# Optimization experiments

Measured on AMD Instinct MI355X. Metric: run time of the kernel, lower is better.

## Reference

```python
import jax, jax.numpy as jnp
import numpy as np

D_MODEL = 1024
N_HEADS = 16
D_FF = 4096
EPS = 1e-6


def _linear_params(key, d_in, d_out):
    kw, kb = jax.random.split(key)
    bound = 1.0 / np.sqrt(d_in)
    W = jax.random.uniform(kw, (d_out, d_in), minval=-bound, maxval=bound, dtype=jnp.float32)
    b = jax.random.uniform(kb, (d_out,), minval=-bound, maxval=bound, dtype=jnp.float32)
    return W, b


def setup_inputs() -> dict:
    key = jax.random.key(0)
    keys = jax.random.split(key, 8)
    x = jax.random.normal(keys[0], (4, 2048, D_MODEL), dtype=jnp.float32)
    mask = jnp.ones((4, 1, 1, 2048), dtype=jnp.bool_)
    Wq, bq = _linear_params(keys[1], D_MODEL, D_MODEL)
    Wk, bk = _linear_params(keys[2], D_MODEL, D_MODEL)
    Wv, bv = _linear_params(keys[3], D_MODEL, D_MODEL)
    Wo, bo = _linear_params(keys[4], D_MODEL, D_MODEL)
    W1, b1 = _linear_params(keys[5], D_MODEL, D_FF)
    W2, b2 = _linear_params(keys[6], D_FF, D_MODEL)
    ln1_g = jnp.ones((D_MODEL,), jnp.float32); ln1_b = jnp.zeros((D_MODEL,), jnp.float32)
    ln2_g = jnp.ones((D_MODEL,), jnp.float32); ln2_b = jnp.zeros((D_MODEL,), jnp.float32)
    return {"x": x, "mask": mask,
            "Wq": Wq, "bq": bq, "Wk": Wk, "bk": bk, "Wv": Wv, "bv": bv,
            "Wo": Wo, "bo": bo, "W1": W1, "b1": b1, "W2": W2, "b2": b2,
            "ln1_g": ln1_g, "ln1_b": ln1_b, "ln2_g": ln2_g, "ln2_b": ln2_b}


def _layernorm(x, g, b):
    # torch LayerNorm here uses unbiased std and divides by (std + eps)
    mean = jnp.mean(x, axis=-1, keepdims=True)
    std = jnp.std(x, axis=-1, keepdims=True, ddof=1)
    return g * (x - mean) / (std + EPS) + b


def _gelu_tanh(x):
    c = np.sqrt(2.0 / np.pi).astype(np.float32)
    return 0.5 * x * (1.0 + jnp.tanh(c * (x + 0.044715 * x * x * x)))


def _mha(xn, mask, Wq, bq, Wk, bk, Wv, bv, Wo, bo):
    B, S, D = xn.shape
    d_k = D // N_HEADS
    def proj(W, b):
        y = jnp.einsum('bsd,ed->bse', xn, W) + b
        return y.reshape(B, S, N_HEADS, d_k).transpose(0, 2, 1, 3)  # [B,h,S,d_k]
    q, k, v = proj(Wq, bq), proj(Wk, bk), proj(Wv, bv)
    scores = jnp.einsum('bhqd,bhkd->bhqk', q, k) / np.float32(np.sqrt(d_k))
    scores = jnp.where(mask, scores, jnp.float32(-1e9))
    p = jax.nn.softmax(scores, axis=-1)
    o = jnp.einsum('bhqk,bhkd->bhqd', p, v)
    o = o.transpose(0, 2, 1, 3).reshape(B, S, D)
    return jnp.einsum('bsd,ed->bse', o, Wo) + bo


def reference(x, mask, Wq, bq, Wk, bk, Wv, bv, Wo, bo, W1, b1, W2, b2,
              ln1_g, ln1_b, ln2_g, ln2_b):
    xn = _layernorm(x, ln1_g, ln1_b)
    y = x + _mha(xn, mask, Wq, bq, Wk, bk, Wv, bv, Wo, bo)
    yn = _layernorm(y, ln2_g, ln2_b)
    h = _gelu_tanh(jnp.einsum('bsd,fd->bsf', yn, W1) + b1)
    z = y + (jnp.einsum('bsf,df->bsd', h, W2) + b2)
    return z
```

## Files before the change

kernel.cpp:

```cpp
#include <hip/hip_runtime.h>

typedef __bf16 bf16;
typedef __bf16 bfx4 __attribute__((ext_vector_type(4)));
typedef __bf16 bfx8 __attribute__((ext_vector_type(8)));
typedef float  fx4  __attribute__((ext_vector_type(4)));

#define NTOK 8192
#define DM   1024
#define DFF  4096
#define SEQ  2048
#define NH   16
#define DK   64

#define OFF_WQKV 0ull
#define OFF_WO   (OFF_WQKV + 3072ull*1024*2)
#define OFF_W1   (OFF_WO   + 1024ull*1024*2)
#define OFF_W2   (OFF_W1   + 4096ull*1024*2)
#define OFF_BQKV (OFF_W2   + 4096ull*1024*2)
#define OFF_XN   (OFF_BQKV + 3072ull*4)
#define OFF_QKV  (OFF_XN   + 8192ull*1024*2)
#define OFF_ATTN (OFF_QKV  + 8192ull*3072*2)
#define OFF_Y    (OFF_ATTN + 8192ull*1024*2)
#define OFF_VT   OFF_Y
#define OFF_H    OFF_XN
#define OFF_YN   OFF_ATTN

__device__ __forceinline__ void gload16(const void* g, void* l) {
  __builtin_amdgcn_global_load_lds(
      (__attribute__((address_space(1))) void*)(g),
      (__attribute__((address_space(3))) void*)(l), 16, 0, 0);
}

__device__ __forceinline__ float gelu_tanh(float x) {
  float u = 0.7978845608028654f * (x + 0.044715f * x * x * x);
  float t = 1.f - 2.f / (__expf(2.f * u) + 1.f);
  return 0.5f * x * (1.f + t);
}

__global__ __launch_bounds__(256) void cast_all(const float* __restrict__ Wq,
                                                const float* __restrict__ Wk,
                                                const float* __restrict__ Wv,
                                                const float* __restrict__ Wo,
                                                const float* __restrict__ W1,
                                                const float* __restrict__ W2,
                                                bf16* __restrict__ dst) {
  const int bid = blockIdx.x;
  const int g = bid >> 9;
  const int j = ((bid & 511) << 11) + threadIdx.x * 8;
  const float* s;
  if (g == 0) s = Wq;
  else if (g == 1) s = Wk;
  else if (g == 2) s = Wv;
  else if (g == 3) s = Wo;
  else if (g < 8) s = W1 + (size_t)(g - 4) * 1048576;
  else s = W2 + (size_t)(g - 8) * 1048576;
  const float4 a = *(const float4*)(s + j);
  const float4 c = *(const float4*)(s + j + 4);
  bfx8 o;
  o[0] = (bf16)a.x; o[1] = (bf16)a.y; o[2] = (bf16)a.z; o[3] = (bf16)a.w;
  o[4] = (bf16)c.x; o[5] = (bf16)c.y; o[6] = (bf16)c.z; o[7] = (bf16)c.w;
  *(bfx8*)(dst + (size_t)g * 1048576 + j) = o;
}

__global__ void biask(const float* __restrict__ bq, const float* __restrict__ bk,
                      const float* __restrict__ bv, float* __restrict__ o) {
  const int i = blockIdx.x * 1024 + threadIdx.x;
  const float* s = blockIdx.x == 0 ? bq : (blockIdx.x == 1 ? bk : bv);
  o[i] = s[threadIdx.x];
}

__global__ __launch_bounds__(256) void ln_kernel(const float* __restrict__ x,
                                                 const float* __restrict__ g,
                                                 const float* __restrict__ b,
                                                 bf16* __restrict__ out) {
  const int row = blockIdx.x;
  const int c = threadIdx.x * 4;
  const float4 v = *(const float4*)&x[(size_t)row * DM + c];
  float s1 = v.x + v.y + v.z + v.w;
  float s2 = v.x * v.x + v.y * v.y + v.z * v.z + v.w * v.w;
  #pragma unroll
  for (int o = 32; o; o >>= 1) { s1 += __shfl_xor(s1, o); s2 += __shfl_xor(s2, o); }
  __shared__ float red[8];
  const int wid = threadIdx.x >> 6;
  if ((threadIdx.x & 63) == 0) { red[wid] = s1; red[4 + wid] = s2; }
  __syncthreads();
  s1 = red[0] + red[1] + red[2] + red[3];
  s2 = red[4] + red[5] + red[6] + red[7];
  const float mean = s1 * (1.f / (float)DM);
  const float var = (s2 - (float)DM * mean * mean) * (1.f / (float)(DM - 1));
  const float inv = 1.f / (sqrtf(fmaxf(var, 0.f)) + 1e-6f);
  bfx4 o;
  o[0] = (bf16)(g[c + 0] * (v.x - mean) * inv + b[c + 0]);
  o[1] = (bf16)(g[c + 1] * (v.y - mean) * inv + b[c + 1]);
  o[2] = (bf16)(g[c + 2] * (v.z - mean) * inv + b[c + 2]);
  o[3] = (bf16)(g[c + 3] * (v.w - mean) * inv + b[c + 3]);
  *(bfx4*)&out[(size_t)row * DM + c] = o;
}

template <int EPI, int VSPLIT>
__global__ __launch_bounds__(256, 2) void gemmk(const bf16* __restrict__ A,
                                                const bf16* __restrict__ B,
                                                const float* __restrict__ bias,
                                                const float* __restrict__ resid,
                                                bf16* __restrict__ vt,
                                                void* __restrict__ outp,
                                                int M, int N, int K) {
  extern __shared__ char lds[];
  const int tid = threadIdx.x;
  const int lane = tid & 63, w = tid >> 6;
  const int l15 = lane & 15, lhi = lane >> 4;
  const int wm = w >> 1, wn = w & 1;

  const int gy = gridDim.y;
  const int nwg = gridDim.x * gy;
  const int L = blockIdx.y * gridDim.x + blockIdx.x;
  const int wid = (L & 7) * (nwg >> 3) + (L >> 3);
  const int m0 = (wid / gy) * 256;
  const int n0 = (wid % gy) * 128;
  const size_t str = (size_t)K * 2;

  const int rT = tid >> 2;
  const int cT = ((tid & 3) ^ ((tid >> 3) & 3)) * 16;
  const char* aS = (const char*)A + (size_t)(m0 + rT) * str + cT;
  const char* bS = (const char*)B + (size_t)(n0 + rT) * str + cT;

  auto stage = [&](int buf, int kt) {
    const size_t kb = (size_t)kt * 64;
    char* d = lds + buf * 24576 + tid * 16;
    #pragma unroll
    for (int p = 0; p < 4; ++p)
      gload16(aS + (size_t)(p * 64) * str + kb, d + p * 4096);
    #pragma unroll
    for (int p = 0; p < 2; ++p)
      gload16(bS + (size_t)(p * 64) * str + kb, d + 16384 + p * 4096);
  };

  fx4 acc[8][4] = {};
  const int nK = K >> 5;

  stage(0, 0);
  stage(1, 1);

  #pragma unroll 1
  for (int t = 0; t < nK; ++t) {
    if (t < nK - 1)
      asm volatile("s_waitcnt vmcnt(6) lgkmcnt(0)" ::: "memory");
    else
      asm volatile("s_waitcnt vmcnt(0) lgkmcnt(0)" ::: "memory");
    __builtin_amdgcn_s_barrier();
    asm volatile("" ::: "memory");
    if (t + 2 < nK) stage((t + 2) % 3, t + 2);

    const char* Ab = lds + (t % 3) * 24576;
    const char* Bb = Ab + 16384;
    bfx8 af[8], bv[4];
    #pragma unroll
    for (int i = 0; i < 8; ++i) {
      const int r = wm * 128 + i * 16 + l15;
      af[i] = *(const bfx8*)(Ab + r * 64 + ((lhi * 16) ^ (((r >> 1) & 3) << 4)));
    }
    #pragma unroll
    for (int j = 0; j < 4; ++j) {
      const int r = wn * 64 + j * 16 + l15;
      bv[j] = *(const bfx8*)(Bb + r * 64 + ((lhi * 16) ^ (((r >> 1) & 3) << 4)));
    }
    __builtin_amdgcn_s_setprio(1);
    #pragma unroll
    for (int i = 0; i < 8; ++i)
      #pragma unroll
      for (int j = 0; j < 4; ++j)
        acc[i][j] = __builtin_amdgcn_mfma_f32_16x16x32_bf16(af[i], bv[j], acc[i][j], 0, 0, 0);
    __builtin_amdgcn_s_setprio(0);
  }

  const int rb = m0 + wm * 128 + lhi * 4;
  const int cb = n0 + wn * 64 + l15;
  #pragma unroll
  for (int j = 0; j < 4; ++j) {
    const int c = cb + j * 16;
    const float bvv = bias[c];
    if (VSPLIT && c >= 2048) {
      const int hd = c - 2048;
      #pragma unroll
      for (int i = 0; i < 8; ++i) {
        const int tok = rb + i * 16;
        const int bb = tok >> 11;
        bfx4 o4;
        #pragma unroll
        for (int e = 0; e < 4; ++e) o4[e] = (bf16)(acc[i][j][e] + bvv);
        *(bfx4*)&vt[((size_t)(bb * 1024 + hd)) * SEQ + (tok & 2047)] = o4;
      }
    } else {
      #pragma unroll
      for (int i = 0; i < 8; ++i) {
        #pragma unroll
        for (int e = 0; e < 4; ++e) {
          const size_t idx = (size_t)(rb + i * 16 + e) * N + c;
          float v = acc[i][j][e] + bvv;
          if constexpr (EPI == 1) v = gelu_tanh(v);
          if constexpr (EPI == 2) {
            ((float*)outp)[idx] = v + resid[idx];
          } else {
            ((bf16*)outp)[idx] = (bf16)v;
          }
        }
      }
    }
  }
}

__global__ __launch_bounds__(256, 4) void attn_kernel(const bf16* __restrict__ QKV,
                                                      const bf16* __restrict__ VT,
                                                      bf16* __restrict__ O) {
  __shared__ bf16 lds[2][2][4096];
  const int tid = threadIdx.x;
  const int lane = tid & 63, w = tid >> 6;
  const int l15 = lane & 15, lhi = lane >> 4;
  int id = blockIdx.x;
  id = (id & 7) * 128 + (id >> 3);
  const int q0 = (id & 15) * 128;
  const int h = (id >> 4) & 15;
  const int b = id >> 8;
  const size_t tokbase = (size_t)b * SEQ;

  const int lin0 = w * 1024 + lane * 16;
  const int lin1 = lin0 + 4096;
  const int row0 = lin0 >> 7, row1 = lin1 >> 7;
  const int cs0 = (lin0 & 127) ^ ((row0 & 7) << 4);
  const int cs1 = (lin1 & 127) ^ ((row1 & 7) << 4);
  const char* kp0 = (const char*)QKV + ((tokbase + row0) * 3072 + 1024 + h * 64) * 2 + cs0;
  const char* kp1 = (const char*)QKV + ((tokbase + row1) * 3072 + 1024 + h * 64) * 2 + cs1;
  const char* vbase = (const char*)(VT + (size_t)((b * NH + h) * 64) * SEQ);
  const char* vp0 = vbase + (size_t)row0 * (SEQ * 2) + cs0;
  const char* vp1 = vbase + (size_t)row1 * (SEQ * 2) + cs1;
  char* const ldsb = (char*)&lds[0][0][0];
  int dofs = 0;
  const long KADV = 64l * 3072 * 2;
  const long VADV = 64l * 2;

  auto stage = [&]() {
    gload16(kp0, ldsb + dofs + lin0);
    gload16(kp1, ldsb + dofs + lin1);
    gload16(vp0, ldsb + dofs + 8192 + lin0);
    gload16(vp1, ldsb + dofs + 8192 + lin1);
    kp0 += KADV; kp1 += KADV; vp0 += VADV; vp1 += VADV;
    dofs ^= 16384;
  };

  stage();

  bfx8 qf[2][2];
  #pragma unroll
  for (int m = 0; m < 2; ++m)
    #pragma unroll
    for (int kk = 0; kk < 2; ++kk) {
      bfx8 raw = *(const bfx8*)&QKV[(tokbase + q0 + w * 32 + m * 16 + l15) * 3072
                                    + h * DK + kk * 32 + lhi * 8];
      bfx8 sc;
      #pragma unroll
      for (int e = 0; e < 8; ++e) sc[e] = (bf16)((float)raw[e] * 0.18033688011112042f);
      qf[m][kk] = sc;
    }

  fx4 acc[2][4] = {};
  fx4 lsum[2] = {};
  bfx8 ones;
  #pragma unroll
  for (int e = 0; e < 8; ++e) ones[e] = (bf16)1.0f;

  const int NT = SEQ / 64;
  #pragma unroll 2
  for (int t = 0; t < NT; ++t) {
    if (t + 1 < NT) {
      stage();
      asm volatile("s_waitcnt vmcnt(4)" ::: "memory");
    } else {
      asm volatile("s_waitcnt vmcnt(0)" ::: "memory");
    }
    __builtin_amdgcn_s_barrier();

    const char* Kl = ldsb + ((t & 1) << 14);
    const char* Vl = Kl + 8192;

    fx4 s[2][4] = {};
    #pragma unroll
    for (int kk = 0; kk < 2; ++kk) {
      bfx8 kf[4];
      #pragma unroll
      for (int n = 0; n < 4; ++n) {
        const int row = n * 16 + l15;
        kf[n] = *(const bfx8*)(Kl + row * 128 + ((kk * 64 + lhi * 16) ^ ((row & 7) << 4)));
      }
      __builtin_amdgcn_s_setprio(1);
      #pragma unroll
      for (int m = 0; m < 2; ++m)
        #pragma unroll
        for (int n = 0; n < 4; ++n)
          s[m][n] = __builtin_amdgcn_mfma_f32_16x16x32_bf16(kf[n], qf[m][kk], s[m][n], 0, 0, 0);
      __builtin_amdgcn_s_setprio(0);
    }

    uint32_t pu[2][4][2];
    #pragma unroll
    for (int m = 0; m < 2; ++m)
      #pragma unroll
      for (int n = 0; n < 4; ++n) {
        const float p0 = exp2f(s[m][n][0]);
        const float p1 = exp2f(s[m][n][1]);
        const float p2 = exp2f(s[m][n][2]);
        const float p3 = exp2f(s[m][n][3]);
        union { bf16 h2[2]; uint32_t u; } c0, c1;
        c0.h2[0] = (bf16)p0; c0.h2[1] = (bf16)p1;
        c1.h2[0] = (bf16)p2; c1.h2[1] = (bf16)p3;
        pu[m][n][0] = c0.u; pu[m][n][1] = c1.u;
      }

    #pragma unroll
    for (int kk = 0; kk < 2; ++kk) {
      bfx8 pB[2];
      #pragma unroll
      for (int m = 0; m < 2; ++m) {
        union { uint32_t u[4]; bfx8 v; } cb2;
        cb2.u[0] = pu[m][2 * kk][0];
        cb2.u[1] = pu[m][2 * kk][1];
        cb2.u[2] = pu[m][2 * kk + 1][0];
        cb2.u[3] = pu[m][2 * kk + 1][1];
        pB[m] = cb2.v;
      }
      __builtin_amdgcn_s_setprio(1);
      #pragma unroll
      for (int m = 0; m < 2; ++m)
        lsum[m] = __builtin_amdgcn_mfma_f32_16x16x32_bf16(ones, pB[m], lsum[m], 0, 0, 0);
      __builtin_amdgcn_s_setprio(0);
      #pragma unroll
      for (int dn = 0; dn < 4; ++dn) {
        const int row = dn * 16 + l15;
        const int sw = (row & 7) << 4;
        union { bfx4 q2[2]; bfx8 v; } vv;
        vv.q2[0] = *(const bfx4*)(Vl + row * 128 + ((kk * 64 + lhi * 8) ^ sw));
        vv.q2[1] = *(const bfx4*)(Vl + row * 128 + ((kk * 64 + 32 + lhi * 8) ^ sw));
        __builtin_amdgcn_s_setprio(1);
        #pragma unroll
        for (int m = 0; m < 2; ++m)
          acc[m][dn] = __builtin_amdgcn_mfma_f32_16x16x32_bf16(vv.v, pB[m], acc[m][dn], 0, 0, 0);
        __builtin_amdgcn_s_setprio(0);
      }
    }

    asm volatile("s_waitcnt lgkmcnt(0)" ::: "memory");
    __builtin_amdgcn_s_barrier();
  }

  __syncthreads();
  bf16* Ep = &lds[0][0][0] + w * 2048;
  const float rinv0 = __builtin_amdgcn_rcpf(lsum[0][0]);
  const float rinv1 = __builtin_amdgcn_rcpf(lsum[1][0]);
  #pragma unroll
  for (int m = 0; m < 2; ++m) {
    const int qr = m * 16 + l15;
    const int sw = (qr & 7) << 4;
    const float ri = m ? rinv1 : rinv0;
    #pragma unroll
    for (int dn = 0; dn < 4; ++dn)
      #pragma unroll
      for (int e = 0; e < 4; ++e) {
        const int d = dn * 16 + lhi * 4 + e;
        *(bf16*)((char*)Ep + qr * 128 + ((2 * d) ^ sw)) = (bf16)(acc[m][dn][e] * ri);
      }
  }
  __syncthreads();
  #pragma unroll
  for (int j = 0; j < 4; ++j) {
    const int qr = lane >> 1;
    const int cbyte = (lane & 1) * 64 + j * 16;
    bfx8 v = *(const bfx8*)((char*)Ep + qr * 128 + (cbyte ^ ((qr & 7) << 4)));
    *(bfx8*)&O[(tokbase + q0 + w * 32 + qr) * (size_t)DM + h * DK + (lane & 1) * 32 + j * 8] = v;
  }
}

extern "C" void kernel_launch(void* const* d_in, const int* in_sizes, int n_in,
                              void* d_out, int out_size, void* d_ws, size_t ws_size,
                              hipStream_t stream) {
  const float* x  = (const float*)d_in[0];
  const float* Wq = (const float*)d_in[2];
  const float* bq = (const float*)d_in[3];
  const float* Wk = (const float*)d_in[4];
  const float* bk = (const float*)d_in[5];
  const float* Wv = (const float*)d_in[6];
  const float* bv = (const float*)d_in[7];
  const float* Wo = (const float*)d_in[8];
  const float* bo = (const float*)d_in[9];
  const float* W1 = (const float*)d_in[10];
  const float* b1 = (const float*)d_in[11];
  const float* W2 = (const float*)d_in[12];
  const float* b2 = (const float*)d_in[13];
  const float* g1 = (const float*)d_in[14];
  const float* be1 = (const float*)d_in[15];
  const float* g2 = (const float*)d_in[16];
  const float* be2 = (const float*)d_in[17];

  char* ws = (char*)d_ws;
  bf16* WQKVb = (bf16*)(ws + OFF_WQKV);
  bf16* WOb   = (bf16*)(ws + OFF_WO);
  bf16* W1b   = (bf16*)(ws + OFF_W1);
  bf16* W2b   = (bf16*)(ws + OFF_W2);
  float* BQKV = (float*)(ws + OFF_BQKV);
  bf16* XN    = (bf16*)(ws + OFF_XN);
  bf16* QKVb  = (bf16*)(ws + OFF_QKV);
  bf16* ATTNb = (bf16*)(ws + OFF_ATTN);
  float* Yb   = (float*)(ws + OFF_Y);
  bf16* VTb   = (bf16*)(ws + OFF_VT);
  bf16* Hb    = (bf16*)(ws + OFF_H);
  bf16* YNb   = (bf16*)(ws + OFF_YN);

  hipFuncSetAttribute((const void*)&gemmk<0, 1>,
                      hipFuncAttributeMaxDynamicSharedMemorySize, 73728);
  hipFuncSetAttribute((const void*)&gemmk<1, 0>,
                      hipFuncAttributeMaxDynamicSharedMemorySize, 73728);
  hipFuncSetAttribute((const void*)&gemmk<2, 0>,
                      hipFuncAttributeMaxDynamicSharedMemorySize, 73728);

  cast_all<<<6144, 256, 0, stream>>>(Wq, Wk, Wv, Wo, W1, W2, WQKVb);
  biask<<<3, 1024, 0, stream>>>(bq, bk, bv, BQKV);

  ln_kernel<<<NTOK, 256, 0, stream>>>(x, g1, be1, XN);
  gemmk<0, 1><<<dim3(32, 24), 256, 73728, stream>>>(XN, WQKVb, BQKV, nullptr,
                                                    VTb, QKVb, NTOK, 3072, 1024);
  attn_kernel<<<1024, 256, 0, stream>>>(QKVb, VTb, ATTNb);
  gemmk<2, 0><<<dim3(32, 8), 256, 73728, stream>>>(ATTNb, WOb, bo, x, nullptr,
                                                   Yb, NTOK, 1024, 1024);
  ln_kernel<<<NTOK, 256, 0, stream>>>(Yb, g2, be2, YNb);
  gemmk<1, 0><<<dim3(32, 32), 256, 73728, stream>>>(YNb, W1b, b1, nullptr,
                                                    nullptr, Hb, NTOK, 4096, 1024);
  gemmk<2, 0><<<dim3(32, 8), 256, 73728, stream>>>(Hb, W2b, b2, Yb, nullptr,
                                                   (float*)d_out, NTOK, 1024, 4096);
}
```

Measured before the change: 440.1 us.

## Double K tile to 64 with two-stage buffering and compile-time GEMM shapes

The GEMM K-step grows from 32 to 64 elements per stage, with an 8-way XOR swizzle over 128-byte LDS rows. It drops the three-buffer, two-ahead prefetch for two buffers with one stage in flight, and adds a second barrier per iteration. Each GEMM becomes its own kernel with constant M/N/K and launch_bounds(256,1), raising LDS per block to 96 KB. This halves loop and barrier overhead per unit of work and lets the compiler specialise the shapes, but it reduces prefetch depth and likely occupancy.

```diff
diff --git a/kernel.cpp b/kernel.cpp
--- a/kernel.cpp
+++ b/kernel.cpp
@@ -98,14 +98,13 @@
 }
 
 template <int EPI, int VSPLIT>
-__global__ __launch_bounds__(256, 2) void gemmk(const bf16* __restrict__ A,
-                                                const bf16* __restrict__ B,
-                                                const float* __restrict__ bias,
-                                                const float* __restrict__ resid,
-                                                bf16* __restrict__ vt,
-                                                void* __restrict__ outp,
-                                                int M, int N, int K) {
-  extern __shared__ char lds[];
+__device__ __forceinline__ void gemm_body(const bf16* __restrict__ A,
+                                          const bf16* __restrict__ B,
+                                          const float* __restrict__ bias,
+                                          const float* __restrict__ resid,
+                                          bf16* __restrict__ vt,
+                                          void* __restrict__ outp,
+                                          int M, int N, int K, char* lds) {
   const int tid = threadIdx.x;
   const int lane = tid & 63, w = tid >> 6;
   const int l15 = lane & 15, lhi = lane >> 4;
@@ -119,58 +118,62 @@
   const int n0 = (wid % gy) * 128;
   const size_t str = (size_t)K * 2;
 
-  const int rT = tid >> 2;
-  const int cT = ((tid & 3) ^ ((tid >> 3) & 3)) * 16;
+  const int rT = tid >> 3;
+  const int cT = ((tid & 7) ^ (rT & 7)) * 16;
   const char* aS = (const char*)A + (size_t)(m0 + rT) * str + cT;
   const char* bS = (const char*)B + (size_t)(n0 + rT) * str + cT;
 
   auto stage = [&](int buf, int kt) {
-    const size_t kb = (size_t)kt * 64;
-    char* d = lds + buf * 24576 + tid * 16;
+    const size_t kb = (size_t)kt * 128;
+    char* d = lds + buf * 49152 + tid * 16;
+    #pragma unroll
+    for (int p = 0; p < 8; ++p)
+      gload16(aS + (size_t)(p * 32) * str + kb, d + p * 4096);
     #pragma unroll
     for (int p = 0; p < 4; ++p)
-      gload16(aS + (size_t)(p * 64) * str + kb, d + p * 4096);
-    #pragma unroll
-    for (int p = 0; p < 2; ++p)
-      gload16(bS + (size_t)(p * 64) * str + kb, d + 16384 + p * 4096);
+      gload16(bS + (size_t)(p * 32) * str + kb, d + 32768 + p * 4096);
   };
 
   fx4 acc[8][4] = {};
-  const int nK = K >> 5;
+  const int asw = (l15 & 7) << 4;
+  const int nK = K >> 6;
 
   stage(0, 0);
-  stage(1, 1);
 
   #pragma unroll 1
   for (int t = 0; t < nK; ++t) {
-    if (t < nK - 1)
-      asm volatile("s_waitcnt vmcnt(6) lgkmcnt(0)" ::: "memory");
-    else
-      asm volatile("s_waitcnt vmcnt(0) lgkmcnt(0)" ::: "memory");
+    asm volatile("s_waitcnt lgkmcnt(0)" ::: "memory");
     __builtin_amdgcn_s_barrier();
     asm volatile("" ::: "memory");
-    if (t + 2 < nK) stage((t + 2) % 3, t + 2);
-
-    const char* Ab = lds + (t % 3) * 24576;
-    const char* Bb = Ab + 16384;
-    bfx8 af[8], bv[4];
-    #pragma unroll
-    for (int i = 0; i < 8; ++i) {
-      const int r = wm * 128 + i * 16 + l15;
-      af[i] = *(const bfx8*)(Ab + r * 64 + ((lhi * 16) ^ (((r >> 1) & 3) << 4)));
-    }
-    #pragma unroll
-    for (int j = 0; j < 4; ++j) {
-      const int r = wn * 64 + j * 16 + l15;
-      bv[j] = *(const bfx8*)(Bb + r * 64 + ((lhi * 16) ^ (((r >> 1) & 3) << 4)));
-    }
-    __builtin_amdgcn_s_setprio(1);
-    #pragma unroll
-    for (int i = 0; i < 8; ++i)
+    if (t + 1 < nK) stage((t + 1) & 1, t + 1);
+    if (t + 1 < nK)
+      asm volatile("s_waitcnt vmcnt(12)" ::: "memory");
+    else
+      asm volatile("s_waitcnt vmcnt(0)" ::: "memory");
+    __builtin_amdgcn_s_barrier();
+    asm volatile("" ::: "memory");
+
+    const char* Ab = lds + (t & 1) * 49152;
+    const char* Bb = Ab + 32768;
+    #pragma unroll
+    for (int kk = 0; kk < 2; ++kk) {
+      bfx8 af[8], bv[4];
+      #pragma unroll
+      for (int i = 0; i < 8; ++i)
+        af[i] = *(const bfx8*)(Ab + (wm * 128 + i * 16 + l15) * 128 +
+                               ((kk * 64 + lhi * 16) ^ asw));
       #pragma unroll
       for (int j = 0; j < 4; ++j)
-        acc[i][j] = __builtin_amdgcn_mfma_f32_16x16x32_bf16(af[i], bv[j], acc[i][j], 0, 0, 0);
-    __builtin_amdgcn_s_setprio(0);
+        bv[j] = *(const bfx8*)(Bb + (wn * 64 + j * 16 + l15) * 128 +
+                               ((kk * 64 + lhi * 16) ^ asw));
+      __builtin_amdgcn_s_setprio(1);
+      #pragma unroll
+      for (int i = 0; i < 8; ++i)
+        #pragma unroll
+        for (int j = 0; j < 4; ++j)
+          acc[i][j] = __builtin_amdgcn_mfma_f32_16x16x32_bf16(af[i], bv[j], acc[i][j], 0, 0, 0);
+      __builtin_amdgcn_s_setprio(0);
+    }
   }
 
   const int rb = m0 + wm * 128 + lhi * 4;
@@ -207,6 +210,30 @@
       }
     }
   }
+}
+
+__global__ __launch_bounds__(256, 1) void g_qkv(const bf16* A, const bf16* B,
+                                                const float* bias, bf16* vt,
+                                                void* outp) {
+  extern __shared__ char lds[];
+  gemm_body<0, 1>(A, B, bias, nullptr, vt, outp, NTOK, 3072, 1024, lds);
+}
+__global__ __launch_bounds__(256, 1) void g_oproj(const bf16* A, const bf16* B,
+                                                  const float* bias, const float* resid,
+                                                  void* outp) {
+  extern __shared__ char lds[];
+  gemm_body<2, 0>(A, B, bias, resid, nullptr, outp, NTOK, 1024, 1024, lds);
+}
+__global__ __launch_bounds__(256, 1) void g_ffn1(const bf16* A, const bf16* B,
+                                                 const float* bias, void* outp) {
+  extern __shared__ char lds[];
+  gemm_body<1, 0>(A, B, bias, nullptr, nullptr, outp, NTOK, 4096, 1024, lds);
+}
+__global__ __launch_bounds__(256, 1) void g_ffn2(const bf16* A, const bf16* B,
+                                                 const float* bias, const float* resid,
+                                                 void* outp) {
+  extern __shared__ char lds[];
+  gemm_body<2, 0>(A, B, bias, resid, nullptr, outp, NTOK, 1024, 4096, lds);
 }
 
 __global__ __launch_bounds__(256, 4) void attn_kernel(const bf16* __restrict__ QKV,
@@ -413,25 +440,23 @@
   bf16* Hb    = (bf16*)(ws + OFF_H);
   bf16* YNb   = (bf16*)(ws + OFF_YN);
 
-  hipFuncSetAttribute((const void*)&gemmk<0, 1>,
-                      hipFuncAttributeMaxDynamicSharedMemorySize, 73728);
-  hipFuncSetAttribute((const void*)&gemmk<1, 0>,
-                      hipFuncAttributeMaxDynamicSharedMemorySize, 73728);
-  hipFuncSetAttribute((const void*)&gemmk<2, 0>,
-                      hipFuncAttributeMaxDynamicSharedMemorySize, 73728);
+  hipFuncSetAttribute((const void*)&g_qkv,
+                      hipFuncAttributeMaxDynamicSharedMemorySize, 98304);
+  hipFuncSetAttribute((const void*)&g_oproj,
+                      hipFuncAttributeMaxDynamicSharedMemorySize, 98304);
+  hipFuncSetAttribute((const void*)&g_ffn1,
+                      hipFuncAttributeMaxDynamicSharedMemorySize, 98304);
+  hipFuncSetAttribute((const void*)&g_ffn2,
+                      hipFuncAttributeMaxDynamicSharedMemorySize, 98304);
 
   cast_all<<<6144, 256, 0, stream>>>(Wq, Wk, Wv, Wo, W1, W2, WQKVb);
   biask<<<3, 1024, 0, stream>>>(bq, bk, bv, BQKV);
 
   ln_kernel<<<NTOK, 256, 0, stream>>>(x, g1, be1, XN);
-  gemmk<0, 1><<<dim3(32, 24), 256, 73728, stream>>>(XN, WQKVb, BQKV, nullptr,
-                                                    VTb, QKVb, NTOK, 3072, 1024);
+  g_qkv<<<dim3(32, 24), 256, 98304, stream>>>(XN, WQKVb, BQKV, VTb, QKVb);
   attn_kernel<<<1024, 256, 0, stream>>>(QKVb, VTb, ATTNb);
-  gemmk<2, 0><<<dim3(32, 8), 256, 73728, stream>>>(ATTNb, WOb, bo, x, nullptr,
-                                                   Yb, NTOK, 1024, 1024);
+  g_oproj<<<dim3(32, 8), 256, 98304, stream>>>(ATTNb, WOb, bo, x, Yb);
   ln_kernel<<<NTOK, 256, 0, stream>>>(Yb, g2, be2, YNb);
-  gemmk<1, 0><<<dim3(32, 32), 256, 73728, stream>>>(YNb, W1b, b1, nullptr,
-                                                    nullptr, Hb, NTOK, 4096, 1024);
-  gemmk<2, 0><<<dim3(32, 8), 256, 73728, stream>>>(Hb, W2b, b2, Yb, nullptr,
-                                                   (float*)d_out, NTOK, 1024, 4096);
-}
+  g_ffn1<<<dim3(32, 32), 256, 98304, stream>>>(YNb, W1b, b1, Hb);
+  g_ffn2<<<dim3(32, 8), 256, 98304, stream>>>(Hb, W2b, b2, Yb, (float*)d_out);
+}
```

Measured after the change: 450.4 us. 1.02x slower.
